# Kernel optimization log

Hardware: AMD Instinct MI355X
Metric: run time of the kernel (lower is better)

Reference implementation:

```python
import jax, jax.numpy as jnp
import numpy as np

B, H, W, C = 32, 256, 256, 3
KH, KW, F = 5, 5, 8


def setup_inputs() -> dict:
    key = jax.random.key(0)
    k1, k2 = jax.random.split(key)
    x = jax.random.normal(k1, (B, H, W, C), dtype=jnp.float32)
    # learned structuring elements, shape (KH, KW, C, F) per build()
    kernel = jax.random.normal(k2, (KH, KW, C, F), dtype=jnp.float32) * 0.1
    return {"x": x, "kernel": kernel}


def _max_of_erosions(x, kernel):
    # tf.nn.erosion2d semantics: out[b,y,x,c] = min_{dy,dx} in[b, y+dy-pt, x+dx-pl, c]
    #                                               - kernel[KH-1-dy, KW-1-dx, c]
    # (erosion = -dilation(-x, reversed kernel)); then channel-max per filter.
    Bq, Hq, Wq, Cq = x.shape
    kh, kw, _, nf = kernel.shape
    pad_h, pad_w = kh - 1, kw - 1          # stride 1, rate 1, SAME padding
    pt, pl = pad_h // 2, pad_w // 2
    xp = jnp.pad(x, ((0, 0), (pt, pad_h - pt), (pl, pad_w - pl), (0, 0)),
                 constant_values=jnp.inf)   # +inf is identity for min
    kflip = kernel[::-1, ::-1]              # reflected structuring element
    ero = None                              # running min over window taps
    for dy in range(kh):                    # small fixed 5x5 tap loop
        for dx in range(kw):
            win = xp[:, dy:dy + Hq, dx:dx + Wq, :]          # [B,H,W,C]
            cand = win[..., None] - kflip[dy, dx]           # [B,H,W,C,F]
            ero = cand if ero is None else jnp.minimum(ero, cand)
    return jnp.max(ero, axis=3)             # channel max -> [B,H,W,F]


def reference(x, kernel):
    return _max_of_erosions(x, kernel)
```

## Files before the change

### kernel.cpp

```cpp
#include <hip/hip_runtime.h>
#include <math.h>


typedef _Float16 h2 __attribute__((ext_vector_type(2)));

static __device__ __forceinline__ h2 cvt_pk(float a, float b) {
    return __builtin_bit_cast(h2, __builtin_amdgcn_cvt_pkrtz(a, b));
}
static __device__ __forceinline__ h2 u2h(unsigned u) {
    return __builtin_bit_cast(h2, u);
}

#define Hq 256
#define RST 132
#define PST (8 * RST)
#define TILE_H2 (3 * PST)
#define INF2 0x7C007C00u

__global__ __launch_bounds__(256) void maxero_pp(
    const float* __restrict__ x,
    const float* __restrict__ kern,
    float* __restrict__ out)
{
    __shared__ __align__(16) h2 xp[TILE_H2];
    __shared__ __align__(16) h2 kd[600];

    const int tid = threadIdx.x;
    const int bI  = blockIdx.x;
    const int b   = bI >> 6;
    const int h0  = (bI & 63) << 2;

    for (int i = tid; i < 600; i += 256) {
        int tap = i / 24, rem = i - tap * 24;
        int c = rem >> 3, f = rem & 7;
        int dy = tap / 5, dx = tap - dy * 5;
        float v = kern[((4 - dy) * 5 + (4 - dx)) * 24 + c * 8 + f];
        kd[i] = cvt_pk(v, v);
    }

    const float* xb = x + (size_t)b * (Hq * 256 * 3);
    #pragma unroll
    for (int k = 0; k < 2; ++k) {
        int g   = tid + k * 256;
        int rr  = g >> 6;
        int pg  = g & 63;
        int r   = h0 - 2 + rr;
        bool rv = (unsigned)r < (unsigned)Hq;
        int rc  = min(max(r, 0), Hq - 1);
        const float4* gp = reinterpret_cast<const float4*>(xb + rc * 768 + pg * 12);
        float4 v0 = gp[0], v1 = gp[1], v2 = gp[2];
        const float fv[12] = { v0.x, v0.y, v0.z, v0.w,
                               v1.x, v1.y, v1.z, v1.w,
                               v2.x, v2.y, v2.z, v2.w };
        int base = rr * RST + 2 * pg + 1;
        #pragma unroll
        for (int c = 0; c < 3; ++c) {
            xp[c * PST + base + 0] = rv ? cvt_pk(fv[c],     fv[3 + c]) : u2h(INF2);
            xp[c * PST + base + 1] = rv ? cvt_pk(fv[6 + c], fv[9 + c]) : u2h(INF2);
        }
    }
    if (tid < 48) {
        int c = tid >> 4, rem = tid & 15;
        int rr = rem >> 1, side = rem & 1;
        xp[c * PST + rr * RST + (side ? 129 : 0)] = u2h(INF2);
    }
    __syncthreads();

    const int hrow = tid >> 6;
    const int w0   = (tid & 63) << 2;

    h2 e01[3][8], e23[3][8];
    #pragma unroll
    for (int c = 0; c < 3; ++c)
        #pragma unroll
        for (int f = 0; f < 8; ++f) {
            e01[c][f] = u2h(INF2);
            e23[c][f] = u2h(INF2);
        }

    #pragma unroll
    for (int dy = 0; dy < 5; ++dy) {
        unsigned a[3][4], mis[3][3];
        #pragma unroll
        for (int c = 0; c < 3; ++c) {
            const h2* xr = &xp[c * PST + (hrow + dy) * RST + (w0 >> 1)];
            uint2 u0 = *reinterpret_cast<const uint2*>(xr);
            uint2 u1 = *reinterpret_cast<const uint2*>(xr + 2);
            a[c][0] = u0.x; a[c][1] = u0.y; a[c][2] = u1.x; a[c][3] = u1.y;
            mis[c][0] = __builtin_amdgcn_alignbit(a[c][1], a[c][0], 16);
            mis[c][1] = __builtin_amdgcn_alignbit(a[c][2], a[c][1], 16);
            mis[c][2] = __builtin_amdgcn_alignbit(a[c][3], a[c][2], 16);
        }
        #pragma unroll
        for (int dx = 0; dx < 5; ++dx) {
            #pragma unroll
            for (int c = 0; c < 3; ++c) {
                h2 p01 = u2h((dx & 1) ? mis[c][dx >> 1]       : a[c][dx >> 1]);
                h2 p23 = u2h((dx & 1) ? mis[c][(dx >> 1) + 1] : a[c][(dx >> 1) + 1]);
                const uint4* kk = reinterpret_cast<const uint4*>(
                    &kd[(dy * 5 + dx) * 24 + c * 8]);
                uint4 k0 = kk[0], k1 = kk[1];
                const unsigned kf[8] = { k0.x, k0.y, k0.z, k0.w,
                                         k1.x, k1.y, k1.z, k1.w };
                #pragma unroll
                for (int f = 0; f < 8; ++f) {
                    e01[c][f] = __builtin_elementwise_min(e01[c][f], p01 - u2h(kf[f]));
                    e23[c][f] = __builtin_elementwise_min(e23[c][f], p23 - u2h(kf[f]));
                }
            }
        }
    }

    float o0[8], o1[8], o2[8], o3[8];
    #pragma unroll
    for (int f = 0; f < 8; ++f) {
        h2 m01 = __builtin_elementwise_max(
                     __builtin_elementwise_max(e01[0][f], e01[1][f]), e01[2][f]);
        h2 m23 = __builtin_elementwise_max(
                     __builtin_elementwise_max(e23[0][f], e23[1][f]), e23[2][f]);
        o0[f] = (float)m01[0]; o1[f] = (float)m01[1];
        o2[f] = (float)m23[0]; o3[f] = (float)m23[1];
    }
    const size_t rowbase = (size_t)b * 65536 + (size_t)(h0 + hrow) * 256 + w0;
    float* op = out + rowbase * 8;
    reinterpret_cast<float4*>(op)[0] = make_float4(o0[0], o0[1], o0[2], o0[3]);
    reinterpret_cast<float4*>(op)[1] = make_float4(o0[4], o0[5], o0[6], o0[7]);
    reinterpret_cast<float4*>(op)[2] = make_float4(o1[0], o1[1], o1[2], o1[3]);
    reinterpret_cast<float4*>(op)[3] = make_float4(o1[4], o1[5], o1[6], o1[7]);
    reinterpret_cast<float4*>(op)[4] = make_float4(o2[0], o2[1], o2[2], o2[3]);
    reinterpret_cast<float4*>(op)[5] = make_float4(o2[4], o2[5], o2[6], o2[7]);
    reinterpret_cast<float4*>(op)[6] = make_float4(o3[0], o3[1], o3[2], o3[3]);
    reinterpret_cast<float4*>(op)[7] = make_float4(o3[4], o3[5], o3[6], o3[7]);
}

extern "C" void kernel_launch(void* const* d_in, const int* in_sizes, int n_in,
                              void* d_out, int out_size, void* d_ws, size_t ws_size,
                              hipStream_t stream) {
    const float* x    = (const float*)d_in[0];
    const float* kern = (const float*)d_in[1];
    float* out        = (float*)d_out;
    maxero_pp<<<2048, 256, 0, stream>>>(x, kern, out);
}
```

Before: 51.41 us.

## Split into pad/pack pre-pass and direct global-read erosion kernel

Adds a pre-pass kernel that converts the input to packed fp16 channel planes with +inf borders in the workspace. The main kernel then reads its window rows straight from global memory (through cache) instead of staging a shared-memory tile, and remaps block indices so blocks are spread across XCDs. The aim is to remove the per-block staging, halo handling and conversion from the compute kernel. In exchange it adds a second launch and an extra write and read of the packed input through global memory.

```diff
diff --git a/kernel.cpp b/kernel.cpp
--- a/kernel.cpp
+++ b/kernel.cpp
@@ -4,70 +4,83 @@
 
 typedef _Float16 h2 __attribute__((ext_vector_type(2)));
 
-static __device__ __forceinline__ h2 cvt_pk(float a, float b) {
-    return __builtin_bit_cast(h2, __builtin_amdgcn_cvt_pkrtz(a, b));
-}
 static __device__ __forceinline__ h2 u2h(unsigned u) {
     return __builtin_bit_cast(h2, u);
 }
+static __device__ __forceinline__ unsigned packh(float a, float b) {
+    return __builtin_bit_cast(unsigned, __builtin_amdgcn_cvt_pkrtz(a, b));
+}
 
-#define Hq 256
-#define RST 132
-#define PST (8 * RST)
-#define TILE_H2 (3 * PST)
 #define INF2 0x7C007C00u
+#define PROW 132
+#define PPLANE (260 * 132)
 
-__global__ __launch_bounds__(256) void maxero_pp(
-    const float* __restrict__ x,
+__global__ __launch_bounds__(256) void pad_pack(
+    const float* __restrict__ x, unsigned* __restrict__ ws)
+{
+    const int tid = threadIdx.x;
+    const int blk = blockIdx.x;
+    if (blk < 2048) {
+        const int b = blk >> 6;
+        const int r = ((blk & 63) << 2) + (tid >> 6);
+        const int g = tid & 63;
+        const float4* p = reinterpret_cast<const float4*>(
+            x + ((size_t)b * 65536 + (size_t)r * 256 + 4 * g) * 3);
+        float4 v0 = p[0], v1 = p[1], v2 = p[2];
+        const float fv[12] = { v0.x, v0.y, v0.z, v0.w,
+                               v1.x, v1.y, v1.z, v1.w,
+                               v2.x, v2.y, v2.z, v2.w };
+        #pragma unroll
+        for (int c = 0; c < 3; ++c) {
+            size_t idx = (size_t)(b * 3 + c) * PPLANE + (size_t)(r + 2) * PROW
+                         + 2 * g + 1;
+            ws[idx]     = packh(fv[c],     fv[3 + c]);
+            ws[idx + 1] = packh(fv[6 + c], fv[9 + c]);
+        }
+    } else {
+        const int b = blk - 2048;
+        for (int i = tid; i < 3120; i += 256) {
+            int c = i / 1040, rm = i - c * 1040;
+            int row, idx;
+            if (rm < 528) {
+                int rr = rm / 132;
+                row = (rr < 2) ? rr : rr + 256;
+                idx = rm - rr * 132;
+            } else {
+                int t = rm - 528;
+                row = 2 + (t >> 1);
+                idx = (t & 1) ? 129 : 0;
+            }
+            ws[(size_t)(b * 3 + c) * PPLANE + (size_t)row * PROW + idx] = INF2;
+        }
+    }
+}
+
+__global__ __launch_bounds__(256) void maxero_direct(
+    const unsigned* __restrict__ ws,
     const float* __restrict__ kern,
     float* __restrict__ out)
 {
-    __shared__ __align__(16) h2 xp[TILE_H2];
-    __shared__ __align__(16) h2 kd[600];
+    __shared__ __align__(16) unsigned kd[600];
 
-    const int tid = threadIdx.x;
-    const int bI  = blockIdx.x;
-    const int b   = bI >> 6;
-    const int h0  = (bI & 63) << 2;
+    const int tid  = threadIdx.x;
+    const int orig = blockIdx.x;
+    const int L    = (orig & 7) * 256 + (orig >> 3);
+    const int b    = L >> 6;
+    const int h0   = (L & 63) << 2;
 
     for (int i = tid; i < 600; i += 256) {
         int tap = i / 24, rem = i - tap * 24;
         int c = rem >> 3, f = rem & 7;
         int dy = tap / 5, dx = tap - dy * 5;
         float v = kern[((4 - dy) * 5 + (4 - dx)) * 24 + c * 8 + f];
-        kd[i] = cvt_pk(v, v);
-    }
-
-    const float* xb = x + (size_t)b * (Hq * 256 * 3);
-    #pragma unroll
-    for (int k = 0; k < 2; ++k) {
-        int g   = tid + k * 256;
-        int rr  = g >> 6;
-        int pg  = g & 63;
-        int r   = h0 - 2 + rr;
-        bool rv = (unsigned)r < (unsigned)Hq;
-        int rc  = min(max(r, 0), Hq - 1);
-        const float4* gp = reinterpret_cast<const float4*>(xb + rc * 768 + pg * 12);
-        float4 v0 = gp[0], v1 = gp[1], v2 = gp[2];
-        const float fv[12] = { v0.x, v0.y, v0.z, v0.w,
-                               v1.x, v1.y, v1.z, v1.w,
-                               v2.x, v2.y, v2.z, v2.w };
-        int base = rr * RST + 2 * pg + 1;
-        #pragma unroll
-        for (int c = 0; c < 3; ++c) {
-            xp[c * PST + base + 0] = rv ? cvt_pk(fv[c],     fv[3 + c]) : u2h(INF2);
-            xp[c * PST + base + 1] = rv ? cvt_pk(fv[6 + c], fv[9 + c]) : u2h(INF2);
-        }
-    }
-    if (tid < 48) {
-        int c = tid >> 4, rem = tid & 15;
-        int rr = rem >> 1, side = rem & 1;
-        xp[c * PST + rr * RST + (side ? 129 : 0)] = u2h(INF2);
+        kd[i] = packh(v, v);
     }
     __syncthreads();
 
     const int hrow = tid >> 6;
     const int w0   = (tid & 63) << 2;
+    const int h    = h0 + hrow;
 
     h2 e01[3][8], e23[3][8];
     #pragma unroll
@@ -78,14 +91,16 @@
             e23[c][f] = u2h(INF2);
         }
 
+    const unsigned* wb = ws + (size_t)b * 3 * PPLANE + (size_t)h * PROW + (w0 >> 1);
+
     #pragma unroll
     for (int dy = 0; dy < 5; ++dy) {
         unsigned a[3][4], mis[3][3];
         #pragma unroll
         for (int c = 0; c < 3; ++c) {
-            const h2* xr = &xp[c * PST + (hrow + dy) * RST + (w0 >> 1)];
-            uint2 u0 = *reinterpret_cast<const uint2*>(xr);
-            uint2 u1 = *reinterpret_cast<const uint2*>(xr + 2);
+            const unsigned* rp = wb + (size_t)c * PPLANE + (size_t)dy * PROW;
+            uint2 u0 = *reinterpret_cast<const uint2*>(rp);
+            uint2 u1 = *reinterpret_cast<const uint2*>(rp + 2);
             a[c][0] = u0.x; a[c][1] = u0.y; a[c][2] = u1.x; a[c][3] = u1.y;
             mis[c][0] = __builtin_amdgcn_alignbit(a[c][1], a[c][0], 16);
             mis[c][1] = __builtin_amdgcn_alignbit(a[c][2], a[c][1], 16);
@@ -121,7 +136,7 @@
         o0[f] = (float)m01[0]; o1[f] = (float)m01[1];
         o2[f] = (float)m23[0]; o3[f] = (float)m23[1];
     }
-    const size_t rowbase = (size_t)b * 65536 + (size_t)(h0 + hrow) * 256 + w0;
+    const size_t rowbase = (size_t)b * 65536 + (size_t)h * 256 + w0;
     float* op = out + rowbase * 8;
     reinterpret_cast<float4*>(op)[0] = make_float4(o0[0], o0[1], o0[2], o0[3]);
     reinterpret_cast<float4*>(op)[1] = make_float4(o0[4], o0[5], o0[6], o0[7]);
@@ -139,5 +154,7 @@
     const float* x    = (const float*)d_in[0];
     const float* kern = (const float*)d_in[1];
     float* out        = (float*)d_out;
-    maxero_pp<<<2048, 256, 0, stream>>>(x, kern, out);
+    unsigned* ws      = (unsigned*)d_ws;
+    pad_pack<<<2080, 256, 0, stream>>>(x, ws);
+    maxero_direct<<<2048, 256, 0, stream>>>(ws, kern, out);
 }
```

After: 61.53 us. 19.7% more time.

## Make blocks persistent over 16 rows with double-buffered LDS prefetch

Applied to the files above, without the earlier changes.

Each block now handles 16 output rows in four 4-row steps instead of one 4-row tile, with 512 blocks instead of 2048. The next step's input rows are loaded into registers before the current step's compute and written into an alternate LDS buffer afterwards, so global loads overlap the min/max arithmetic. This amortises the kernel-table setup per block and the halo rows are still reloaded. The risk is lower parallelism: 512 blocks may underfill a 256-CU GPU and limit latency hiding, and the dy loop is no longer unrolled.

```diff
diff --git a/kernel.cpp b/kernel.cpp
--- a/kernel.cpp
+++ b/kernel.cpp
@@ -4,133 +4,167 @@
 
 typedef _Float16 h2 __attribute__((ext_vector_type(2)));
 
-static __device__ __forceinline__ h2 cvt_pk(float a, float b) {
-    return __builtin_bit_cast(h2, __builtin_amdgcn_cvt_pkrtz(a, b));
-}
 static __device__ __forceinline__ h2 u2h(unsigned u) {
     return __builtin_bit_cast(h2, u);
 }
+static __device__ __forceinline__ unsigned packh(float a, float b) {
+    return __builtin_bit_cast(unsigned, __builtin_amdgcn_cvt_pkrtz(a, b));
+}
 
-#define Hq 256
 #define RST 132
 #define PST (8 * RST)
-#define TILE_H2 (3 * PST)
+#define TILE_U (3 * PST)
 #define INF2 0x7C007C00u
 
-__global__ __launch_bounds__(256) void maxero_pp(
+__global__ __launch_bounds__(256) void maxero_pipe(
     const float* __restrict__ x,
     const float* __restrict__ kern,
     float* __restrict__ out)
 {
-    __shared__ __align__(16) h2 xp[TILE_H2];
-    __shared__ __align__(16) h2 kd[600];
+    __shared__ __align__(16) unsigned xp[2][TILE_U];
+    __shared__ __align__(16) unsigned kd[600];
 
     const int tid = threadIdx.x;
     const int bI  = blockIdx.x;
-    const int b   = bI >> 6;
-    const int h0  = (bI & 63) << 2;
+    const int b   = bI >> 4;
+    const int seg = bI & 15;
 
     for (int i = tid; i < 600; i += 256) {
         int tap = i / 24, rem = i - tap * 24;
         int c = rem >> 3, f = rem & 7;
         int dy = tap / 5, dx = tap - dy * 5;
         float v = kern[((4 - dy) * 5 + (4 - dx)) * 24 + c * 8 + f];
-        kd[i] = cvt_pk(v, v);
+        kd[i] = packh(v, v);
     }
 
-    const float* xb = x + (size_t)b * (Hq * 256 * 3);
+    const float* xb = x + (size_t)b * (256 * 256 * 3);
+    const int rr0 = tid >> 6;
+    const int pg  = tid & 63;
+    const int hrow = rr0;
+    const int w0   = pg << 2;
+
+    float4 pv[6]; bool prv[2];
     #pragma unroll
     for (int k = 0; k < 2; ++k) {
-        int g   = tid + k * 256;
-        int rr  = g >> 6;
-        int pg  = g & 63;
-        int r   = h0 - 2 + rr;
-        bool rv = (unsigned)r < (unsigned)Hq;
-        int rc  = min(max(r, 0), Hq - 1);
+        int r  = seg * 16 - 2 + rr0 + k * 4;
+        prv[k] = (unsigned)r < 256u;
+        int rc = min(max(r, 0), 255);
         const float4* gp = reinterpret_cast<const float4*>(xb + rc * 768 + pg * 12);
-        float4 v0 = gp[0], v1 = gp[1], v2 = gp[2];
-        const float fv[12] = { v0.x, v0.y, v0.z, v0.w,
-                               v1.x, v1.y, v1.z, v1.w,
-                               v2.x, v2.y, v2.z, v2.w };
-        int base = rr * RST + 2 * pg + 1;
+        pv[k*3+0] = gp[0]; pv[k*3+1] = gp[1]; pv[k*3+2] = gp[2];
+    }
+    #pragma unroll
+    for (int k = 0; k < 2; ++k) {
+        int base = (rr0 + k * 4) * RST + 2 * pg + 1;
+        float4 v0 = pv[k*3], v1 = pv[k*3+1], v2 = pv[k*3+2];
+        const float fv[12] = { v0.x,v0.y,v0.z,v0.w, v1.x,v1.y,v1.z,v1.w,
+                               v2.x,v2.y,v2.z,v2.w };
         #pragma unroll
         for (int c = 0; c < 3; ++c) {
-            xp[c * PST + base + 0] = rv ? cvt_pk(fv[c],     fv[3 + c]) : u2h(INF2);
-            xp[c * PST + base + 1] = rv ? cvt_pk(fv[6 + c], fv[9 + c]) : u2h(INF2);
+            xp[0][c*PST + base]     = prv[k] ? packh(fv[c],   fv[3+c]) : INF2;
+            xp[0][c*PST + base + 1] = prv[k] ? packh(fv[6+c], fv[9+c]) : INF2;
         }
     }
     if (tid < 48) {
-        int c = tid >> 4, rem = tid & 15;
-        int rr = rem >> 1, side = rem & 1;
-        xp[c * PST + rr * RST + (side ? 129 : 0)] = u2h(INF2);
+        int c = tid >> 4, rem = tid & 15, rr = rem >> 1, side = rem & 1;
+        xp[0][c*PST + rr*RST + (side ? 129 : 0)] = INF2;
     }
     __syncthreads();
 
-    const int hrow = tid >> 6;
-    const int w0   = (tid & 63) << 2;
-
-    h2 e01[3][8], e23[3][8];
-    #pragma unroll
-    for (int c = 0; c < 3; ++c)
-        #pragma unroll
-        for (int f = 0; f < 8; ++f) {
-            e01[c][f] = u2h(INF2);
-            e23[c][f] = u2h(INF2);
+    #pragma unroll 1
+    for (int t = 0; t < 4; ++t) {
+        float4 nv[6]; bool nrv[2];
+        if (t < 3) {
+            #pragma unroll
+            for (int k = 0; k < 2; ++k) {
+                int r  = seg * 16 + (t + 1) * 4 - 2 + rr0 + k * 4;
+                nrv[k] = (unsigned)r < 256u;
+                int rc = min(max(r, 0), 255);
+                const float4* gp = reinterpret_cast<const float4*>(xb + rc*768 + pg*12);
+                nv[k*3+0] = gp[0]; nv[k*3+1] = gp[1]; nv[k*3+2] = gp[2];
+            }
         }
 
-    #pragma unroll
-    for (int dy = 0; dy < 5; ++dy) {
-        unsigned a[3][4], mis[3][3];
+        const unsigned* cb = xp[t & 1];
+        h2 e01[3][8], e23[3][8];
         #pragma unroll
-        for (int c = 0; c < 3; ++c) {
-            const h2* xr = &xp[c * PST + (hrow + dy) * RST + (w0 >> 1)];
-            uint2 u0 = *reinterpret_cast<const uint2*>(xr);
-            uint2 u1 = *reinterpret_cast<const uint2*>(xr + 2);
-            a[c][0] = u0.x; a[c][1] = u0.y; a[c][2] = u1.x; a[c][3] = u1.y;
-            mis[c][0] = __builtin_amdgcn_alignbit(a[c][1], a[c][0], 16);
-            mis[c][1] = __builtin_amdgcn_alignbit(a[c][2], a[c][1], 16);
-            mis[c][2] = __builtin_amdgcn_alignbit(a[c][3], a[c][2], 16);
-        }
-        #pragma unroll
-        for (int dx = 0; dx < 5; ++dx) {
+        for (int c = 0; c < 3; ++c)
+            #pragma unroll
+            for (int f = 0; f < 8; ++f) { e01[c][f] = u2h(INF2); e23[c][f] = u2h(INF2); }
+
+        #pragma unroll 1
+        for (int dy = 0; dy < 5; ++dy) {
+            unsigned a[3][4], mis[3][3];
             #pragma unroll
             for (int c = 0; c < 3; ++c) {
-                h2 p01 = u2h((dx & 1) ? mis[c][dx >> 1]       : a[c][dx >> 1]);
-                h2 p23 = u2h((dx & 1) ? mis[c][(dx >> 1) + 1] : a[c][(dx >> 1) + 1]);
-                const uint4* kk = reinterpret_cast<const uint4*>(
-                    &kd[(dy * 5 + dx) * 24 + c * 8]);
-                uint4 k0 = kk[0], k1 = kk[1];
-                const unsigned kf[8] = { k0.x, k0.y, k0.z, k0.w,
-                                         k1.x, k1.y, k1.z, k1.w };
+                const unsigned* xr = &cb[c*PST + (hrow + dy)*RST + (w0 >> 1)];
+                uint2 u0 = *reinterpret_cast<const uint2*>(xr);
+                uint2 u1 = *reinterpret_cast<const uint2*>(xr + 2);
+                a[c][0] = u0.x; a[c][1] = u0.y; a[c][2] = u1.x; a[c][3] = u1.y;
+                mis[c][0] = __builtin_amdgcn_alignbit(a[c][1], a[c][0], 16);
+                mis[c][1] = __builtin_amdgcn_alignbit(a[c][2], a[c][1], 16);
+                mis[c][2] = __builtin_amdgcn_alignbit(a[c][3], a[c][2], 16);
+            }
+            #pragma unroll
+            for (int dx = 0; dx < 5; ++dx) {
                 #pragma unroll
-                for (int f = 0; f < 8; ++f) {
-                    e01[c][f] = __builtin_elementwise_min(e01[c][f], p01 - u2h(kf[f]));
-                    e23[c][f] = __builtin_elementwise_min(e23[c][f], p23 - u2h(kf[f]));
+                for (int c = 0; c < 3; ++c) {
+                    h2 p01 = u2h((dx & 1) ? mis[c][dx >> 1]     : a[c][dx >> 1]);
+                    h2 p23 = u2h((dx & 1) ? mis[c][(dx >> 1)+1] : a[c][(dx >> 1)+1]);
+                    const uint4* kk = reinterpret_cast<const uint4*>(
+                        &kd[(dy*5 + dx)*24 + c*8]);
+                    uint4 k0 = kk[0], k1 = kk[1];
+                    const unsigned kf[8] = { k0.x,k0.y,k0.z,k0.w,
+                                             k1.x,k1.y,k1.z,k1.w };
+                    #pragma unroll
+                    for (int f = 0; f < 8; ++f) {
+                        e01[c][f] = __builtin_elementwise_min(e01[c][f], p01 - u2h(kf[f]));
+                        e23[c][f] = __builtin_elementwise_min(e23[c][f], p23 - u2h(kf[f]));
+                    }
                 }
             }
         }
+
+        float o0[8], o1[8], o2[8], o3[8];
+        #pragma unroll
+        for (int f = 0; f < 8; ++f) {
+            h2 m01 = __builtin_elementwise_max(
+                         __builtin_elementwise_max(e01[0][f], e01[1][f]), e01[2][f]);
+            h2 m23 = __builtin_elementwise_max(
+                         __builtin_elementwise_max(e23[0][f], e23[1][f]), e23[2][f]);
+            o0[f] = (float)m01[0]; o1[f] = (float)m01[1];
+            o2[f] = (float)m23[0]; o3[f] = (float)m23[1];
+        }
+        float* op = out + ((size_t)b*65536 + (size_t)(seg*16 + t*4 + hrow)*256 + w0) * 8;
+        reinterpret_cast<float4*>(op)[0] = make_float4(o0[0],o0[1],o0[2],o0[3]);
+        reinterpret_cast<float4*>(op)[1] = make_float4(o0[4],o0[5],o0[6],o0[7]);
+        reinterpret_cast<float4*>(op)[2] = make_float4(o1[0],o1[1],o1[2],o1[3]);
+        reinterpret_cast<float4*>(op)[3] = make_float4(o1[4],o1[5],o1[6],o1[7]);
+        reinterpret_cast<float4*>(op)[4] = make_float4(o2[0],o2[1],o2[2],o2[3]);
+        reinterpret_cast<float4*>(op)[5] = make_float4(o2[4],o2[5],o2[6],o2[7]);
+        reinterpret_cast<float4*>(op)[6] = make_float4(o3[0],o3[1],o3[2],o3[3]);
+        reinterpret_cast<float4*>(op)[7] = make_float4(o3[4],o3[5],o3[6],o3[7]);
+
+        if (t < 3) {
+            unsigned* nb = xp[(t + 1) & 1];
+            #pragma unroll
+            for (int k = 0; k < 2; ++k) {
+                int base = (rr0 + k * 4) * RST + 2 * pg + 1;
+                float4 v0 = nv[k*3], v1 = nv[k*3+1], v2 = nv[k*3+2];
+                const float fv[12] = { v0.x,v0.y,v0.z,v0.w, v1.x,v1.y,v1.z,v1.w,
+                                       v2.x,v2.y,v2.z,v2.w };
+                #pragma unroll
+                for (int c = 0; c < 3; ++c) {
+                    nb[c*PST + base]     = nrv[k] ? packh(fv[c],   fv[3+c]) : INF2;
+                    nb[c*PST + base + 1] = nrv[k] ? packh(fv[6+c], fv[9+c]) : INF2;
+                }
+            }
+            if (tid < 48) {
+                int c = tid >> 4, rem = tid & 15, rr = rem >> 1, side = rem & 1;
+                nb[c*PST + rr*RST + (side ? 129 : 0)] = INF2;
+            }
+        }
+        __syncthreads();
     }
-
-    float o0[8], o1[8], o2[8], o3[8];
-    #pragma unroll
-    for (int f = 0; f < 8; ++f) {
-        h2 m01 = __builtin_elementwise_max(
-                     __builtin_elementwise_max(e01[0][f], e01[1][f]), e01[2][f]);
-        h2 m23 = __builtin_elementwise_max(
-                     __builtin_elementwise_max(e23[0][f], e23[1][f]), e23[2][f]);
-        o0[f] = (float)m01[0]; o1[f] = (float)m01[1];
-        o2[f] = (float)m23[0]; o3[f] = (float)m23[1];
-    }
-    const size_t rowbase = (size_t)b * 65536 + (size_t)(h0 + hrow) * 256 + w0;
-    float* op = out + rowbase * 8;
-    reinterpret_cast<float4*>(op)[0] = make_float4(o0[0], o0[1], o0[2], o0[3]);
-    reinterpret_cast<float4*>(op)[1] = make_float4(o0[4], o0[5], o0[6], o0[7]);
-    reinterpret_cast<float4*>(op)[2] = make_float4(o1[0], o1[1], o1[2], o1[3]);
-    reinterpret_cast<float4*>(op)[3] = make_float4(o1[4], o1[5], o1[6], o1[7]);
-    reinterpret_cast<float4*>(op)[4] = make_float4(o2[0], o2[1], o2[2], o2[3]);
-    reinterpret_cast<float4*>(op)[5] = make_float4(o2[4], o2[5], o2[6], o2[7]);
-    reinterpret_cast<float4*>(op)[6] = make_float4(o3[0], o3[1], o3[2], o3[3]);
-    reinterpret_cast<float4*>(op)[7] = make_float4(o3[4], o3[5], o3[6], o3[7]);
 }
 
 extern "C" void kernel_launch(void* const* d_in, const int* in_sizes, int n_in,
@@ -139,5 +173,5 @@
     const float* x    = (const float*)d_in[0];
     const float* kern = (const float*)d_in[1];
     float* out        = (float*)d_out;
-    maxero_pp<<<2048, 256, 0, stream>>>(x, kern, out);
+    maxero_pipe<<<512, 256, 0, stream>>>(x, kern, out);
 }
```

New measurement: 65.23 us. +26.9%, slower.
